# Optimization experiments

Hardware: AMD Instinct MI355X
Metric: run time of the kernel (lower is better)

## Reference

```python
import jax, jax.numpy as jnp
import numpy as np

H = 1024   # hidden_dim
NH = 16    # num_heads
HD = H // NH  # head_dim = 64
B, S = 2, 2048
LN_EPS = 1e-5


def setup_inputs() -> dict:
    key = jax.random.key(0)
    ks = jax.random.split(key, 5)
    scale = 1.0 / np.sqrt(H)  # xavier-ish scale for stability
    return {
        "x": jax.random.normal(ks[0], (B, S, H), dtype=jnp.float32),
        "Wq": jax.random.normal(ks[1], (H, H), dtype=jnp.float32) * scale,
        "bq": jnp.zeros((H,), jnp.float32),
        "Wk": jax.random.normal(ks[2], (H, H), dtype=jnp.float32) * scale,
        "bk": jnp.zeros((H,), jnp.float32),
        "Wv": jax.random.normal(ks[3], (H, H), dtype=jnp.float32) * scale,
        "bv": jnp.zeros((H,), jnp.float32),
        "Wo": jax.random.normal(ks[4], (H, H), dtype=jnp.float32) * scale,
        "bo": jnp.zeros((H,), jnp.float32),
        "ln_gamma": jnp.ones((H,), jnp.float32),
        "ln_beta": jnp.zeros((H,), jnp.float32),
    }


def reference(x, Wq, bq, Wk, bk, Wv, bv, Wo, bo, ln_gamma, ln_beta):
    b, s, _ = x.shape
    # QKV projections, split heads: (b, nh, s, hd)
    def split_heads(t):
        return t.reshape(b, s, NH, HD).transpose(0, 2, 1, 3)
    Q = split_heads(x @ Wq + bq)
    K = split_heads(x @ Wk + bk)
    V = split_heads(x @ Wv + bv)
    # scaled dot-product with clamp (mask=None path)
    scores = jnp.einsum('bhqd,bhkd->bhqk', Q, K) / np.sqrt(HD).astype(np.float32)
    scores = jnp.clip(scores, -10000.0, 10000.0)
    attn = jax.nn.softmax(scores, axis=-1)
    # dropout is identity in eval mode
    ctx = jnp.einsum('bhqk,bhkd->bhqd', attn, V)
    ctx = ctx.transpose(0, 2, 1, 3).reshape(b, s, H)
    out = ctx @ Wo + bo
    # residual + LayerNorm
    y = out + x
    mu = jnp.mean(y, axis=-1, keepdims=True)
    var = jnp.mean(jnp.square(y - mu), axis=-1, keepdims=True)
    y = (y - mu) * jax.lax.rsqrt(var + LN_EPS)
    return y * ln_gamma + ln_beta
```

## Files before the change

### kernel.cpp

```cpp
#include <hip/hip_runtime.h>

typedef unsigned short u16;
typedef __attribute__((ext_vector_type(8))) short shortx8;
typedef __attribute__((ext_vector_type(4))) float floatx4;
typedef __attribute__((ext_vector_type(2))) unsigned uintx2;

#define GLD16(gp, lp) __builtin_amdgcn_global_load_lds( \
    (__attribute__((address_space(1))) void*)(gp), \
    (__attribute__((address_space(3))) void*)(lp), 16, 0, 0)

__device__ __forceinline__ u16 f2bf(float f) {
  union { float f; unsigned u; } v; v.f = f;
  unsigned r = v.u + 0x7FFFu + ((v.u >> 16) & 1u);
  return (u16)(r >> 16);
}

__device__ __forceinline__ unsigned pkbf(float a, float b) {
#if __has_builtin(__builtin_amdgcn_cvt_pk_bf16_f32)
  auto r = __builtin_amdgcn_cvt_pk_bf16_f32(a, b);
  return __builtin_bit_cast(unsigned, r);
#else
  union { float f; unsigned u; } x, y; x.f = a; y.f = b;
  return __builtin_amdgcn_perm(y.u + 0x8000u, x.u + 0x8000u, 0x07060302u);
#endif
}

__global__ __launch_bounds__(256) void prep_kernel(const float* __restrict__ x,
                                                   u16* __restrict__ xb,
                                                   const float* __restrict__ Wq,
                                                   const float* __restrict__ Wk,
                                                   const float* __restrict__ Wv,
                                                   const float* __restrict__ Wo,
                                                   u16* __restrict__ Wt) {
  __shared__ u16 tile[32][33];
  int bid = blockIdx.x;
  int tid = threadIdx.x;
  if (bid < 4096) {
    int i = bid * 256 + tid;
    float4 v = ((const float4*)x)[i];
    uintx2 o;
    o.x = pkbf(v.x, v.y);
    o.y = pkbf(v.z, v.w);
    ((uintx2*)xb)[i] = o;
  } else {
    int block = bid - 4096;
    int mat = block >> 10;
    int rem = block & 1023;
    const float* W = (mat == 0) ? Wq : (mat == 1) ? Wk : (mat == 2) ? Wv : Wo;
    u16* dst = Wt + (size_t)mat * 1024 * 1024;
    int n0 = (rem & 31) * 32, k0 = (rem >> 5) * 32;
    int tx = tid & 31, ty = tid >> 5;
    for (int i = 0; i < 4; ++i)
      tile[ty + i * 8][tx] = f2bf(W[(size_t)(k0 + ty + i * 8) * 1024 + n0 + tx]);
    __syncthreads();
    for (int i = 0; i < 4; ++i)
      dst[(size_t)(n0 + ty + i * 8) * 1024 + k0 + tx] = tile[tx][ty + i * 8];
  }
}

__device__ __forceinline__ void gemm_tile_core(const u16* __restrict__ A,
                                               const u16* __restrict__ Bt,
                                               int m0, int n0,
                                               u16* As, u16* Bs,
                                               floatx4 (&acc)[4][4]) {
  const int tid = threadIdx.x;
  const int wave = tid >> 6, lane = tid & 63;
  const int lrow = lane >> 4, lcol = lane & 15;
  const int wm = wave >> 1, wn = wave & 1;

  for (int mi = 0; mi < 4; ++mi)
    for (int ni = 0; ni < 4; ++ni)
      acc[mi][ni] = (floatx4){0.f, 0.f, 0.f, 0.f};

  const u16* ap[4];
  const u16* bp[4];
  for (int l = 0; l < 4; ++l) {
    int g = (l * 4 + wave) * 64 + lane;
    int r = g >> 3, c = g & 7;
    int cc = (c ^ (r & 7)) * 8;
    ap[l] = A + (size_t)(m0 + r) * 1024 + cc;
    bp[l] = Bt + (size_t)(n0 + r) * 1024 + cc;
  }

  for (int k0 = 0; k0 < 1024; k0 += 64) {
    __syncthreads();
    for (int l = 0; l < 4; ++l) {
      GLD16(ap[l], As + (l * 4 + wave) * 512);
      GLD16(bp[l], Bs + (l * 4 + wave) * 512);
      ap[l] += 64; bp[l] += 64;
    }
    __syncthreads();
    for (int kk = 0; kk < 2; ++kk) {
      shortx8 af[4], bf[4];
      for (int mi = 0; mi < 4; ++mi) {
        int row = wm * 64 + mi * 16 + lcol;
        int gr = (kk * 4 + lrow) ^ (row & 7);
        af[mi] = *(const shortx8*)&As[row * 64 + gr * 8];
      }
      for (int ni = 0; ni < 4; ++ni) {
        int row = wn * 64 + ni * 16 + lcol;
        int gr = (kk * 4 + lrow) ^ (row & 7);
        bf[ni] = *(const shortx8*)&Bs[row * 64 + gr * 8];
      }
      for (int mi = 0; mi < 4; ++mi)
        for (int ni = 0; ni < 4; ++ni)
          acc[mi][ni] = __builtin_amdgcn_mfma_f32_16x16x32_bf16(af[mi], bf[ni], acc[mi][ni], 0, 0, 0);
    }
  }
}

__global__ __launch_bounds__(256) void qkv_gemm(const u16* __restrict__ xb,
                                                const u16* __restrict__ Wt,
                                                const float* __restrict__ bq,
                                                const float* __restrict__ bk,
                                                const float* __restrict__ bv,
                                                u16* __restrict__ Qh,
                                                u16* __restrict__ Kh,
                                                u16* __restrict__ Vth) {
  __shared__ u16 sbuf[128 * 128];
  u16* As = sbuf;
  u16* Bs = sbuf + 128 * 64;
  int m0 = blockIdx.x * 128;
  int mat = blockIdx.y >> 3;
  int n0 = (blockIdx.y & 7) * 128;
  floatx4 acc[4][4];
  gemm_tile_core(xb, Wt + (size_t)mat * 1024 * 1024, m0, n0, As, Bs, acc);

  const float* bias = (mat == 0) ? bq : (mat == 1) ? bk : bv;
  const int tid = threadIdx.x;
  const int wave = tid >> 6, lane = tid & 63;
  const int lrow = lane >> 4, lcol = lane & 15;
  const int wm = wave >> 1, wn = wave & 1;
  const float qscale = 0.18033688011f;

  if (mat < 2) {
    u16* dst = (mat == 0) ? Qh : Kh;
    float sc = (mat == 0) ? qscale : 1.0f;
    __syncthreads();
    for (int mi = 0; mi < 4; ++mi) {
      int mb = wm * 64 + mi * 16 + lrow * 4;
      for (int ni = 0; ni < 4; ++ni) {
        int n = wn * 64 + ni * 16 + lcol;
        float bval = bias[n0 + n];
        for (int r = 0; r < 4; ++r) {
          int m = mb + r;
          sbuf[m * 128 + (((n >> 3) ^ (m & 15)) * 8) + (n & 7)] =
              f2bf((acc[mi][ni][r] + bval) * sc);
        }
      }
    }
    __syncthreads();
    int row = tid >> 1, half = tid & 1;
    int m = m0 + row;
    int bb = m >> 11, s = m & 2047;
    for (int i = 0; i < 8; ++i) {
      int cg = half * 8 + i;
      int pg = cg ^ (row & 15);
      shortx8 v = *(const shortx8*)&sbuf[row * 128 + pg * 8];
      int ng = n0 + cg * 8;
      int h = ng >> 6, d = ng & 63;
      *(shortx8*)&dst[((size_t)(bb * 16 + h) * 2048 + s) * 64 + d] = v;
    }
  } else {
    for (int mi = 0; mi < 4; ++mi) {
      int mbase = m0 + wm * 64 + mi * 16 + lrow * 4;
      int bb = mbase >> 11, s = mbase & 2047;
      for (int ni = 0; ni < 4; ++ni) {
        int n = n0 + wn * 64 + ni * 16 + lcol;
        float bval = bias[n];
        int h = n >> 6, d = n & 63;
        uintx2 pk;
        pk.x = pkbf(acc[mi][ni][0] + bval, acc[mi][ni][1] + bval);
        pk.y = pkbf(acc[mi][ni][2] + bval, acc[mi][ni][3] + bval);
        *(uintx2*)&Vth[((size_t)(bb * 16 + h) * 64 + d) * 2048 + s] = pk;
      }
    }
  }
}

__global__ __launch_bounds__(256) void out_gemm(const u16* __restrict__ ctx,
                                                const u16* __restrict__ Wot,
                                                const float* __restrict__ bo,
                                                float* __restrict__ aout) {
  __shared__ u16 As[128 * 64];
  __shared__ u16 Bs[64 * 64];
  int m0 = blockIdx.x * 128;
  int n0 = blockIdx.y * 64;
  const int tid = threadIdx.x;
  const int wave = tid >> 6, lane = tid & 63;
  const int lrow = lane >> 4, lcol = lane & 15;
  const int wm = wave >> 1, wn = wave & 1;

  floatx4 acc[4][2];
  for (int mi = 0; mi < 4; ++mi)
    for (int ni = 0; ni < 2; ++ni)
      acc[mi][ni] = (floatx4){0.f, 0.f, 0.f, 0.f};

  const u16* ap[4];
  const u16* bp[2];
  for (int l = 0; l < 4; ++l) {
    int g = (l * 4 + wave) * 64 + lane;
    int r = g >> 3, c = g & 7;
    ap[l] = ctx + (size_t)(m0 + r) * 1024 + (c ^ (r & 7)) * 8;
  }
  for (int l = 0; l < 2; ++l) {
    int g = (l * 4 + wave) * 64 + lane;
    int r = g >> 3, c = g & 7;
    bp[l] = Wot + (size_t)(n0 + r) * 1024 + (c ^ (r & 7)) * 8;
  }

  for (int k0 = 0; k0 < 1024; k0 += 64) {
    __syncthreads();
    for (int l = 0; l < 4; ++l) { GLD16(ap[l], As + (l * 4 + wave) * 512); ap[l] += 64; }
    for (int l = 0; l < 2; ++l) { GLD16(bp[l], Bs + (l * 4 + wave) * 512); bp[l] += 64; }
    __syncthreads();
    for (int kk = 0; kk < 2; ++kk) {
      shortx8 af[4], bf[2];
      for (int mi = 0; mi < 4; ++mi) {
        int row = wm * 64 + mi * 16 + lcol;
        int gr = (kk * 4 + lrow) ^ (row & 7);
        af[mi] = *(const shortx8*)&As[row * 64 + gr * 8];
      }
      for (int ni = 0; ni < 2; ++ni) {
        int row = wn * 32 + ni * 16 + lcol;
        int gr = (kk * 4 + lrow) ^ (row & 7);
        bf[ni] = *(const shortx8*)&Bs[row * 64 + gr * 8];
      }
      for (int mi = 0; mi < 4; ++mi)
        for (int ni = 0; ni < 2; ++ni)
          acc[mi][ni] = __builtin_amdgcn_mfma_f32_16x16x32_bf16(af[mi], bf[ni], acc[mi][ni], 0, 0, 0);
    }
  }

  for (int mi = 0; mi < 4; ++mi) {
    int mbase = m0 + wm * 64 + mi * 16 + lrow * 4;
    for (int ni = 0; ni < 2; ++ni) {
      int n = n0 + wn * 32 + ni * 16 + lcol;
      float bval = bo[n];
      for (int r = 0; r < 4; ++r)
        aout[(size_t)(mbase + r) * 1024 + n] = acc[mi][ni][r] + bval;
    }
  }
}

__global__ __launch_bounds__(512) void attn_kernel(const u16* __restrict__ Qh,
                                                   const u16* __restrict__ Kh,
                                                   const u16* __restrict__ Vth,
                                                   u16* __restrict__ ctx) {
  __shared__ u16 QPs[128 * 64];
  __shared__ u16 Ks[2][64 * 64];
  __shared__ u16 Vs[2][64 * 64];

  int bh = blockIdx.x;
  int b = bh >> 4, h = bh & 15;
  int q0 = blockIdx.y * 128;
  int tid = threadIdx.x;
  int wave = tid >> 6, lane = tid & 63;
  int lrow = lane >> 4, lcol = lane & 15;

  const u16* Qg = Qh + ((size_t)bh * 2048 + q0) * 64;
  for (int l = 0; l < 2; ++l) {
    int g = (l * 8 + wave) * 64 + lane;
    int r = g >> 3, c = g & 7;
    GLD16(Qg + r * 64 + ((c ^ (r & 7)) * 8), QPs + (l * 8 + wave) * 512);
  }

  const u16* Kbase = Kh + (size_t)bh * 2048 * 64;
  const u16* Vbase = Vth + (size_t)bh * 64 * 2048;

  int g = wave * 64 + lane;
  int gr = g >> 3, gc = g & 7;
  int cc = (gc ^ (gr & 7)) * 8;
  const u16* kp = Kbase + (size_t)gr * 64 + cc;
  const u16* vp = Vbase + (size_t)gr * 2048 + cc;

  GLD16(kp, (u16*)Ks + wave * 512);
  GLD16(vp, (u16*)Vs + wave * 512);
  kp += 4096;
  vp += 64;
  __syncthreads();

  shortx8 qf[2];
  for (int kk = 0; kk < 2; ++kk) {
    int row = wave * 16 + lcol;
    int grr = (kk * 4 + lrow) ^ (row & 7);
    qf[kk] = *(const shortx8*)&QPs[row * 64 + grr * 8];
  }

  const short one_bf = (short)0x3F80;
  const shortx8 ones8 = {one_bf, one_bf, one_bf, one_bf, one_bf, one_bf, one_bf, one_bf};

  floatx4 o[4];
  floatx4 lacc = (floatx4){0.f, 0.f, 0.f, 0.f};
  for (int dt = 0; dt < 4; ++dt) o[dt] = (floatx4){0.f, 0.f, 0.f, 0.f};

  for (int i = 0; i < 32; ++i) {
    int cur = i & 1;
    if (i < 31) {
      GLD16(kp, (u16*)Ks + (cur ^ 1) * 4096 + wave * 512);
      GLD16(vp, (u16*)Vs + (cur ^ 1) * 4096 + wave * 512);
      kp += 4096;
      vp += 64;
    }

    floatx4 sc[4];
    for (int kt = 0; kt < 4; ++kt)
      sc[kt] = (floatx4){0.f, 0.f, 0.f, 0.f};
    for (int kk = 0; kk < 2; ++kk) {
      for (int kt = 0; kt < 4; ++kt) {
        int row = kt * 16 + lcol;
        int grr = (kk * 4 + lrow) ^ (row & 7);
        shortx8 kf = *(const shortx8*)&Ks[cur][row * 64 + grr * 8];
        sc[kt] = __builtin_amdgcn_mfma_f32_16x16x32_bf16(kf, qf[kk], sc[kt], 0, 0, 0);
      }
    }

    {
      int row = wave * 16 + lcol;
      for (int kt = 0; kt < 4; ++kt) {
        float p0 = __builtin_amdgcn_exp2f(sc[kt][0]);
        float p1 = __builtin_amdgcn_exp2f(sc[kt][1]);
        float p2 = __builtin_amdgcn_exp2f(sc[kt][2]);
        float p3 = __builtin_amdgcn_exp2f(sc[kt][3]);
        int gg = kt * 2 + (lrow >> 1);
        int addr = row * 64 + ((gg ^ (row & 7)) * 8) + (lrow & 1) * 4;
        uintx2 pk;
        pk.x = pkbf(p0, p1);
        pk.y = pkbf(p2, p3);
        *(uintx2*)&QPs[addr] = pk;
      }
    }

    for (int kk = 0; kk < 2; ++kk) {
      int prow = wave * 16 + lcol;
      int pgr = (kk * 4 + lrow) ^ (prow & 7);
      shortx8 pf = *(const shortx8*)&QPs[prow * 64 + pgr * 8];
      lacc = __builtin_amdgcn_mfma_f32_16x16x32_bf16(ones8, pf, lacc, 0, 0, 0);
      for (int dt = 0; dt < 4; ++dt) {
        int row = dt * 16 + lcol;
        int grr = (kk * 4 + lrow) ^ (row & 7);
        shortx8 vf = *(const shortx8*)&Vs[cur][row * 64 + grr * 8];
        o[dt] = __builtin_amdgcn_mfma_f32_16x16x32_bf16(vf, pf, o[dt], 0, 0, 0);
      }
    }
    __syncthreads();
  }

  {
    float inv = 1.0f / lacc[0];
    int s = q0 + wave * 16 + lcol;
    u16* dst = ctx + (size_t)(b * 2048 + s) * 1024 + h * 64 + lrow * 4;
    for (int dt = 0; dt < 4; ++dt) {
      uintx2 pk;
      pk.x = pkbf(o[dt][0] * inv, o[dt][1] * inv);
      pk.y = pkbf(o[dt][2] * inv, o[dt][3] * inv);
      *(uintx2*)(dst + dt * 16) = pk;
    }
  }
}

__global__ __launch_bounds__(256) void ln_kernel(const float* __restrict__ aout,
                                                 const float* __restrict__ x,
                                                 const float* __restrict__ gamma,
                                                 const float* __restrict__ beta,
                                                 float* __restrict__ out) {
  int row = blockIdx.x;
  int t = threadIdx.x;
  const float4* a4 = (const float4*)(aout + (size_t)row * 1024);
  const float4* x4 = (const float4*)(x + (size_t)row * 1024);
  float4 v = a4[t];
  float4 xv = x4[t];
  v.x += xv.x; v.y += xv.y; v.z += xv.z; v.w += xv.w;
  float s = v.x + v.y + v.z + v.w;
  float s2 = v.x * v.x + v.y * v.y + v.z * v.z + v.w * v.w;
  for (int off = 1; off < 64; off <<= 1) {
    s += __shfl_xor(s, off, 64);
    s2 += __shfl_xor(s2, off, 64);
  }
  __shared__ float red[8];
  int wave = t >> 6, lane = t & 63;
  if (lane == 0) { red[wave] = s; red[4 + wave] = s2; }
  __syncthreads();
  s = red[0] + red[1] + red[2] + red[3];
  s2 = red[4] + red[5] + red[6] + red[7];
  float mu = s * (1.0f / 1024.0f);
  float var = s2 * (1.0f / 1024.0f) - mu * mu;
  float rstd = rsqrtf(var + 1e-5f);
  float4 g = ((const float4*)gamma)[t];
  float4 be = ((const float4*)beta)[t];
  float4 y;
  y.x = (v.x - mu) * rstd * g.x + be.x;
  y.y = (v.y - mu) * rstd * g.y + be.y;
  y.z = (v.z - mu) * rstd * g.z + be.z;
  y.w = (v.w - mu) * rstd * g.w + be.w;
  ((float4*)(out + (size_t)row * 1024))[t] = y;
}

extern "C" void kernel_launch(void* const* d_in, const int* in_sizes, int n_in,
                              void* d_out, int out_size, void* d_ws, size_t ws_size,
                              hipStream_t stream) {
  const float* x     = (const float*)d_in[0];
  const float* Wq    = (const float*)d_in[1];
  const float* bq    = (const float*)d_in[2];
  const float* Wk    = (const float*)d_in[3];
  const float* bk    = (const float*)d_in[4];
  const float* Wv    = (const float*)d_in[5];
  const float* bv    = (const float*)d_in[6];
  const float* Wo    = (const float*)d_in[7];
  const float* bo    = (const float*)d_in[8];
  const float* gamma = (const float*)d_in[9];
  const float* beta  = (const float*)d_in[10];
  float* out = (float*)d_out;

  char* ws = (char*)d_ws;
  u16* xb   = (u16*)(ws);
  u16* Wt   = (u16*)(ws + ((size_t)8 << 20));
  u16* Qh   = (u16*)(ws + ((size_t)16 << 20));
  u16* Kh   = (u16*)(ws + ((size_t)24 << 20));
  u16* Vth  = (u16*)(ws + ((size_t)32 << 20));
  u16* ctx  = (u16*)(ws + ((size_t)40 << 20));
  float* aout = (float*)(ws + ((size_t)48 << 20));

  prep_kernel<<<8192, 256, 0, stream>>>(x, xb, Wq, Wk, Wv, Wo, Wt);
  qkv_gemm<<<dim3(32, 24), 256, 0, stream>>>(xb, Wt, bq, bk, bv, Qh, Kh, Vth);
  attn_kernel<<<dim3(32, 16), 512, 0, stream>>>(Qh, Kh, Vth, ctx);
  out_gemm<<<dim3(32, 16), 256, 0, stream>>>(ctx, Wt + (size_t)3 * 1024 * 1024, bo, aout);
  ln_kernel<<<4096, 256, 0, stream>>>(aout, x, gamma, beta, out);
}
```

Measured before the change: 205.0 us.

## Keep P in registers, permute V into matching layout, raise MFMA priority

Result: no change. 204.3 us (-0.3%).

```diff
diff --git a/kernel.cpp b/kernel.cpp
--- a/kernel.cpp
+++ b/kernel.cpp
@@ -3,7 +3,9 @@
 typedef unsigned short u16;
 typedef __attribute__((ext_vector_type(8))) short shortx8;
 typedef __attribute__((ext_vector_type(4))) float floatx4;
+typedef __attribute__((ext_vector_type(2))) float floatx2;
 typedef __attribute__((ext_vector_type(2))) unsigned uintx2;
+typedef __attribute__((ext_vector_type(4))) unsigned uintx4;
 
 #define GLD16(gp, lp) __builtin_amdgcn_global_load_lds( \
     (__attribute__((address_space(1))) void*)(gp), \
@@ -272,12 +274,23 @@
   int gr = g >> 3, gc = g & 7;
   int cc = (gc ^ (gr & 7)) * 8;
   const u16* kp = Kbase + (size_t)gr * 64 + cc;
-  const u16* vp = Vbase + (size_t)gr * 2048 + cc;
-
-  GLD16(kp, (u16*)Ks + wave * 512);
-  GLD16(vp, (u16*)Vs + wave * 512);
-  kp += 4096;
-  vp += 64;
+
+  const u16* vp = Vbase + (size_t)gr * 2048 + gc * 8;
+  int hh = gc >> 2, ct = gc & 3;
+  int ua = 4 * (ct & 1) + (ct >> 1);
+  int chunkA = hh * 4 + (ua >> 1);
+  int offA = gr * 128 + ((chunkA ^ (gr & 7)) * 16) + (ua & 1) * 8;
+  int offB = gr * 128 + (((chunkA + 1) ^ (gr & 7)) * 16) + (ua & 1) * 8;
+
+  {
+    float4 vreg = *(const float4*)vp;
+    vp += 64;
+    GLD16(kp, (u16*)Ks + wave * 512);
+    kp += 4096;
+    char* vb = (char*)Vs;
+    *(floatx2*)(vb + offA) = (floatx2){vreg.x, vreg.y};
+    *(floatx2*)(vb + offB) = (floatx2){vreg.z, vreg.w};
+  }
   __syncthreads();
 
   shortx8 qf[2];
@@ -296,16 +309,18 @@
 
   for (int i = 0; i < 32; ++i) {
     int cur = i & 1;
+    float4 vreg;
     if (i < 31) {
+      vreg = *(const float4*)vp;
+      vp += 64;
       GLD16(kp, (u16*)Ks + (cur ^ 1) * 4096 + wave * 512);
-      GLD16(vp, (u16*)Vs + (cur ^ 1) * 4096 + wave * 512);
       kp += 4096;
-      vp += 64;
     }
 
     floatx4 sc[4];
     for (int kt = 0; kt < 4; ++kt)
       sc[kt] = (floatx4){0.f, 0.f, 0.f, 0.f};
+    __builtin_amdgcn_s_setprio(1);
     for (int kk = 0; kk < 2; ++kk) {
       for (int kt = 0; kt < 4; ++kt) {
         int row = kt * 16 + lcol;
@@ -314,35 +329,39 @@
         sc[kt] = __builtin_amdgcn_mfma_f32_16x16x32_bf16(kf, qf[kk], sc[kt], 0, 0, 0);
       }
     }
-
-    {
-      int row = wave * 16 + lcol;
-      for (int kt = 0; kt < 4; ++kt) {
-        float p0 = __builtin_amdgcn_exp2f(sc[kt][0]);
-        float p1 = __builtin_amdgcn_exp2f(sc[kt][1]);
-        float p2 = __builtin_amdgcn_exp2f(sc[kt][2]);
-        float p3 = __builtin_amdgcn_exp2f(sc[kt][3]);
-        int gg = kt * 2 + (lrow >> 1);
-        int addr = row * 64 + ((gg ^ (row & 7)) * 8) + (lrow & 1) * 4;
-        uintx2 pk;
-        pk.x = pkbf(p0, p1);
-        pk.y = pkbf(p2, p3);
-        *(uintx2*)&QPs[addr] = pk;
-      }
-    }
-
+    __builtin_amdgcn_s_setprio(0);
+
+    float p[4][4];
+    for (int kt = 0; kt < 4; ++kt)
+      for (int r = 0; r < 4; ++r)
+        p[kt][r] = __builtin_amdgcn_exp2f(sc[kt][r]);
+    shortx8 pf[2];
     for (int kk = 0; kk < 2; ++kk) {
-      int prow = wave * 16 + lcol;
-      int pgr = (kk * 4 + lrow) ^ (prow & 7);
-      shortx8 pf = *(const shortx8*)&QPs[prow * 64 + pgr * 8];
-      lacc = __builtin_amdgcn_mfma_f32_16x16x32_bf16(ones8, pf, lacc, 0, 0, 0);
+      uintx4 w;
+      w.x = pkbf(p[2 * kk][0], p[2 * kk][1]);
+      w.y = pkbf(p[2 * kk][2], p[2 * kk][3]);
+      w.z = pkbf(p[2 * kk + 1][0], p[2 * kk + 1][1]);
+      w.w = pkbf(p[2 * kk + 1][2], p[2 * kk + 1][3]);
+      pf[kk] = __builtin_bit_cast(shortx8, w);
+    }
+
+    if (i < 31) {
+      char* vb = (char*)Vs + (cur ^ 1) * 8192;
+      *(floatx2*)(vb + offA) = (floatx2){vreg.x, vreg.y};
+      *(floatx2*)(vb + offB) = (floatx2){vreg.z, vreg.w};
+    }
+
+    __builtin_amdgcn_s_setprio(1);
+    for (int kk = 0; kk < 2; ++kk) {
+      lacc = __builtin_amdgcn_mfma_f32_16x16x32_bf16(ones8, pf[kk], lacc, 0, 0, 0);
       for (int dt = 0; dt < 4; ++dt) {
         int row = dt * 16 + lcol;
         int grr = (kk * 4 + lrow) ^ (row & 7);
         shortx8 vf = *(const shortx8*)&Vs[cur][row * 64 + grr * 8];
-        o[dt] = __builtin_amdgcn_mfma_f32_16x16x32_bf16(vf, pf, o[dt], 0, 0, 0);
-      }
-    }
+        o[dt] = __builtin_amdgcn_mfma_f32_16x16x32_bf16(vf, pf[kk], o[dt], 0, 0, 0);
+      }
+    }
+    __builtin_amdgcn_s_setprio(0);
     __syncthreads();
   }
 
```
